# Kernel optimization log

Hardware: AMD Instinct MI355X
Metric: run time of the kernel (lower is better)

Reference implementation:

```python
import jax, jax.numpy as jnp
import numpy as np
from jax import lax

V, D, H, L = 128, 1024, 1024, 2
B, T = 64, 512


def setup_inputs() -> dict:
    key = jax.random.key(0)
    ks = jax.random.split(key, 8)
    s = 0.05
    return {
        "x": jax.random.randint(ks[0], (B, T), 0, V),
        "embed": jax.random.normal(ks[1], (V, D), jnp.float32) * s,
        "Wx": jax.random.normal(ks[2], (L, 4 * H, D), jnp.float32) * s,
        "Wh": jax.random.normal(ks[3], (L, 4 * H, H), jnp.float32) * s,
        "b": jax.random.normal(ks[4], (L, 4 * H), jnp.float32) * s,
        "Wout": jax.random.normal(ks[5], (V, H), jnp.float32) * s,
        "bout": jax.random.normal(ks[6], (V,), jnp.float32) * s,
    }


def _lstm_step(Wx, Wh, b, carry, x_t):
    # carry: (h[L,B,H], c[L,B,H]); x_t: [B,D]
    h, c = carry
    inp = x_t
    hs, cs = [], []
    for l in range(L):
        gates = inp @ Wx[l].T + h[l] @ Wh[l].T + b[l]  # [B,4H]
        i, f, g, o = jnp.split(gates, 4, axis=-1)
        c_new = jax.nn.sigmoid(f) * c[l] + jax.nn.sigmoid(i) * jnp.tanh(g)
        h_new = jax.nn.sigmoid(o) * jnp.tanh(c_new)
        hs.append(h_new)
        cs.append(c_new)
        inp = h_new
    return (jnp.stack(hs), jnp.stack(cs)), inp


def reference(x, embed, Wx, Wh, b, Wout, bout):
    emb = embed[x]                      # [B,T,D]
    xs = jnp.swapaxes(emb, 0, 1)        # [T,B,D] for scan over time
    h0 = jnp.zeros((L, B, H), emb.dtype)
    c0 = jnp.zeros((L, B, H), emb.dtype)
    step = lambda carry, x_t: _lstm_step(Wx, Wh, b, carry, x_t)
    _, outs = lax.scan(step, (h0, c0), xs)  # outs: [T,B,H] (top-layer h)
    outs = jnp.swapaxes(outs, 0, 1)         # [B,T,H]
    logits = outs @ Wout.T + bout           # [B,T,V]
    return logits
```

## Files before the change

kernel.cpp:

```cpp
#include <hip/hip_runtime.h>
#include <hip/hip_bf16.h>

constexpr int cV = 128, cD = 1024, cH = 1024, cB = 64, cT = 512;
constexpr int c4H = 4096;
constexpr int NBLK = 256;
constexpr int FSTR = 32;

typedef __attribute__((ext_vector_type(8))) short bf16x8;
typedef __attribute__((ext_vector_type(4))) float f32x4;
typedef __attribute__((ext_vector_type(4))) int i32x4;

__device__ __forceinline__ short f2b(float f) {
  __hip_bfloat16 h = __float2bfloat16(f);
  return __builtin_bit_cast(short, h);
}
__device__ __forceinline__ float sigf(float x) { return 1.0f / (1.0f + __expf(-x)); }

__device__ __forceinline__ void gload16(const short* g, short* l) {
  __builtin_amdgcn_global_load_lds(
      (const __attribute__((address_space(1))) void*)g,
      (__attribute__((address_space(3))) void*)l, 16, 0, 0);
}

__global__ void cvt_bf16_kernel(const float* __restrict__ src, short* __restrict__ dst, int n8) {
  int q = blockIdx.x * blockDim.x + threadIdx.x;
  if (q >= n8) return;
  const float4* s = (const float4*)src + (size_t)q * 2;
  float4 a = s[0], b = s[1];
  union { short s8[8]; int4 v; } u;
  u.s8[0] = f2b(a.x); u.s8[1] = f2b(a.y); u.s8[2] = f2b(a.z); u.s8[3] = f2b(a.w);
  u.s8[4] = f2b(b.x); u.s8[5] = f2b(b.y); u.s8[6] = f2b(b.z); u.s8[7] = f2b(b.w);
  *(int4*)(dst + (size_t)q * 8) = u.v;
}

struct RParams {
  const float* Wx;
  const float* Wh;
  const float* bias;
  const int*   x;
  const short* embedb;
  short* h0hist;
  short* outs;
  const short* zpage;
  int* flags;
};

__launch_bounds__(512, 1)
__global__ void lstm_recurrent(RParams P) {
  __shared__ __align__(16) short S0[32768];
  __shared__ __align__(16) short S1[32768];
  __shared__ float pLDS[8][32][17];
  __shared__ float cLDS[512];
  __shared__ float bLDS[2][32];
  __shared__ short hLDS[512];

  const int tid = threadIdx.x;
  const int lane = tid & 63, wv = tid >> 6;
  const int l15 = lane & 15, lhi = lane >> 4;
  const int op = wv & 3;
  const int ns = wv >> 2;
  const int blk = blockIdx.x;
  const int slice = blk & 127;
  const int bh = blk >> 7;
  const int hc0 = slice * 8;
  int* F = P.flags;
  const int fbase = bh * 128;

  bf16x8 w[32];
  {
    const float* Wsrc = ((op & 1) ? P.Wh : P.Wx) + (size_t)(op >> 1) * c4H * cD;
    int r = ns * 16 + l15;
    const float* base = Wsrc + (size_t)((r >> 3) * cH + hc0 + (r & 7)) * cD + lhi * 8;
    #pragma unroll
    for (int kt = 0; kt < 32; ++kt) {
      float4 a = *(const float4*)(base + kt * 32);
      float4 b = *(const float4*)(base + kt * 32 + 4);
      union { short s8[8]; bf16x8 v; } u;
      u.s8[0] = f2b(a.x); u.s8[1] = f2b(a.y); u.s8[2] = f2b(a.z); u.s8[3] = f2b(a.w);
      u.s8[4] = f2b(b.x); u.s8[5] = f2b(b.y); u.s8[6] = f2b(b.z); u.s8[7] = f2b(b.w);
      w[kt] = u.v;
    }
  }
  if (tid < 64) {
    int l = tid >> 5, r = tid & 31;
    bLDS[l][r] = P.bias[l * c4H + (r >> 3) * cH + hc0 + (r & 7)];
  }
  cLDS[tid] = 0.0f;
  __syncthreads();

  f32x4 accx[2] = {};
  if (op == 0) {
    int v0 = P.x[(bh * 32 + l15) * cT + 0];
    int v1 = P.x[(bh * 32 + 16 + l15) * cT + 0];
    const short* e0 = P.embedb + (size_t)v0 * 1024 + lhi * 8;
    const short* e1 = P.embedb + (size_t)v1 * 1024 + lhi * 8;
    #pragma unroll
    for (int kt = 0; kt < 32; ++kt) {
      bf16x8 a0 = *(const bf16x8*)(e0 + kt * 32);
      bf16x8 a1 = *(const bf16x8*)(e1 + kt * 32);
      accx[0] = __builtin_amdgcn_mfma_f32_16x16x32_bf16(a0, w[kt], accx[0], 0, 0, 0);
      accx[1] = __builtin_amdgcn_mfma_f32_16x16x32_bf16(a1, w[kt], accx[1], 0, 0, 0);
    }
  }

  for (int p = 0; p <= cT; ++p) {
    const bool l0act = (p < cT);
    const bool l1act = (p >= 1);
    const short* s0g = P.h0hist + (size_t)p * 65536;
    const short* s1g = (p >= 2) ? (P.outs + (size_t)(p - 2) * 65536) : P.zpage;

    if (wv >= 6) {
      const int* fa = &F[(fbase + 2 * lane) * FSTR];
      const int* fb = &F[(fbase + 2 * lane + 1) * FSTR];
      const short* gsrc = (wv == 7) ? s0g : s1g;
      short* ldst = (wv == 7) ? S0 : S1;
      unsigned long long staged = 0ull;
      while (staged != ~0ull) {
        int va = __hip_atomic_load(fa, __ATOMIC_RELAXED, __HIP_MEMORY_SCOPE_AGENT);
        int vb = __hip_atomic_load(fb, __ATOMIC_RELAXED, __HIP_MEMORY_SCOPE_AGENT);
        unsigned long long m = __ballot(va >= p && vb >= p) & ~staged;
        if (!m) { __builtin_amdgcn_s_sleep(1); continue; }
        staged |= m;
        while (m) {
          int c = __builtin_ctzll(m);
          m &= m - 1;
          int oct = 2 * c + (lane >> 5);
          int row = lane & 31;
          gload16(gsrc + oct * 512 + bh * 256 + row * 8, ldst + (c * 64 + lane) * 8);
        }
      }
      asm volatile("s_waitcnt vmcnt(0)" ::: "memory");
    }
    __syncthreads();

    f32x4 acc[2];
    if (op == 0) {
      acc[0] = accx[0]; acc[1] = accx[1];
    } else {
      acc[0] = (f32x4){0.f, 0.f, 0.f, 0.f};
      acc[1] = (f32x4){0.f, 0.f, 0.f, 0.f};
      const short* S = (op == 3) ? S1 : S0;
      const short* lb = S + lhi * 256 + l15 * 8;
      #pragma unroll
      for (int kt = 0; kt < 32; ++kt) {
        bf16x8 a0 = *(const bf16x8*)(lb + kt * 1024);
        bf16x8 a1 = *(const bf16x8*)(lb + kt * 1024 + 128);
        acc[0] = __builtin_amdgcn_mfma_f32_16x16x32_bf16(a0, w[kt], acc[0], 0, 0, 0);
        acc[1] = __builtin_amdgcn_mfma_f32_16x16x32_bf16(a1, w[kt], acc[1], 0, 0, 0);
      }
    }
    #pragma unroll
    for (int mi = 0; mi < 2; ++mi)
      #pragma unroll
      for (int v = 0; v < 4; ++v)
        pLDS[wv][mi * 16 + lhi * 4 + v][l15] = acc[mi][v];
    __syncthreads();

    {
      int l = tid >> 8, b = (tid >> 3) & 31, hc = tid & 7;
      bool act = l ? l1act : l0act;
      if (act) {
        float gt[4];
        #pragma unroll
        for (int g = 0; g < 4; ++g) {
          int r = g * 8 + hc;
          int wB = (r >> 4) * 4 + 2 * l;
          gt[g] = pLDS[wB][b][r & 15] + pLDS[wB + 1][b][r & 15] + bLDS[l][r];
        }
        float cold = cLDS[tid];
        float cn = sigf(gt[1]) * cold + sigf(gt[0]) * tanhf(gt[2]);
        float hn = sigf(gt[3]) * tanhf(cn);
        cLDS[tid] = cn;
        hLDS[tid] = f2b(hn);
      }
    }
    __syncthreads();

    if (wv == 0) {
      bool doStore = (lane < 32) ? l0act : l1act;
      if (doStore) {
        short* d = (lane < 32)
            ? (P.h0hist + (size_t)(p + 1) * 65536 + slice * 512 + bh * 256 + (lane & 31) * 8)
            : (P.outs   + (size_t)(p - 1) * 65536 + slice * 512 + bh * 256 + (lane & 31) * 8);
        i32x4 hv = *(const i32x4*)&hLDS[lane * 8];
        asm volatile("global_store_dwordx4 %0, %1, off sc0 sc1" :: "v"(d), "v"(hv) : "memory");
      }
      asm volatile("s_waitcnt vmcnt(0)" ::: "memory");
      if (lane == 0)
        __hip_atomic_store(&F[blk * FSTR], p + 1, __ATOMIC_RELAXED, __HIP_MEMORY_SCOPE_AGENT);
    }

    if (op == 0) {
      accx[0] = (f32x4){0.f, 0.f, 0.f, 0.f};
      accx[1] = (f32x4){0.f, 0.f, 0.f, 0.f};
      if (p + 1 < cT) {
        int t = p + 1;
        int v0 = P.x[(bh * 32 + l15) * cT + t];
        int v1 = P.x[(bh * 32 + 16 + l15) * cT + t];
        const short* e0 = P.embedb + (size_t)v0 * 1024 + lhi * 8;
        const short* e1 = P.embedb + (size_t)v1 * 1024 + lhi * 8;
        #pragma unroll
        for (int kt = 0; kt < 32; ++kt) {
          bf16x8 a0 = *(const bf16x8*)(e0 + kt * 32);
          bf16x8 a1 = *(const bf16x8*)(e1 + kt * 32);
          accx[0] = __builtin_amdgcn_mfma_f32_16x16x32_bf16(a0, w[kt], accx[0], 0, 0, 0);
          accx[1] = __builtin_amdgcn_mfma_f32_16x16x32_bf16(a1, w[kt], accx[1], 0, 0, 0);
        }
      }
    }
  }
}

__launch_bounds__(256, 1)
__global__ void proj_kernel(const short* __restrict__ outs, const short* __restrict__ Woutb,
                            const float* __restrict__ bout, float* __restrict__ logits) {
  const int tid = threadIdx.x, lane = tid & 63, wv = tid >> 6;
  const int l15 = lane & 15, lhi = lane >> 4;
  const int t = blockIdx.x;
  const int row = wv * 16 + l15;
  const short* Abase = outs + (size_t)t * 65536;
  f32x4 acc[8] = {};
  for (int k = 0; k < 1024; k += 32) {
    bf16x8 af = *(const bf16x8*)(Abase + ((k >> 3) + lhi) * 512 + row * 8);
    #pragma unroll
    for (int nn = 0; nn < 8; ++nn) {
      bf16x8 bf = *(const bf16x8*)(Woutb + (size_t)(nn * 16 + l15) * 1024 + k + lhi * 8);
      acc[nn] = __builtin_amdgcn_mfma_f32_16x16x32_bf16(af, bf, acc[nn], 0, 0, 0);
    }
  }
  #pragma unroll
  for (int nn = 0; nn < 8; ++nn) {
    #pragma unroll
    for (int v = 0; v < 4; ++v) {
      int b = wv * 16 + lhi * 4 + v;
      int col = nn * 16 + l15;
      logits[(size_t)b * (cT * cV) + (size_t)t * cV + col] = acc[nn][v] + bout[col];
    }
  }
}

extern "C" void kernel_launch(void* const* d_in, const int* in_sizes, int n_in,
                              void* d_out, int out_size, void* d_ws, size_t ws_size,
                              hipStream_t stream) {
  const int* x = (const int*)d_in[0];
  const float* embed = (const float*)d_in[1];
  const float* Wx = (const float*)d_in[2];
  const float* Wh = (const float*)d_in[3];
  const float* bias = (const float*)d_in[4];
  const float* Wout = (const float*)d_in[5];
  const float* bout = (const float*)d_in[6];
  float* logits = (float*)d_out;

  char* ws = (char*)d_ws;
  size_t off = 0;
  auto alloc = [&](size_t bytes) {
    char* p = ws + off;
    off += (bytes + 255) & ~(size_t)255;
    return p;
  };
  short* Woutb  = (short*)alloc((size_t)cV * cH * 2);
  short* embedb = (short*)alloc((size_t)cV * cD * 2);
  short* outs   = (short*)alloc((size_t)cT * 65536 * 2);
  short* h0hist = (short*)alloc((size_t)(cT + 1) * 65536 * 2);
  char* state0 = ws + off;
  short* zpage  = (short*)alloc((size_t)65536 * 2);
  int* flags    = (int*)alloc((size_t)NBLK * FSTR * sizeof(int));
  size_t state_bytes = (size_t)((ws + off) - state0);

  hipMemsetAsync(state0, 0, state_bytes, stream);
  hipMemsetAsync(h0hist, 0, (size_t)65536 * 2, stream);

  int n8 = cV * cH / 8;
  cvt_bf16_kernel<<<(n8 + 255) / 256, 256, 0, stream>>>(Wout, Woutb, n8);
  cvt_bf16_kernel<<<(n8 + 255) / 256, 256, 0, stream>>>(embed, embedb, n8);

  RParams P{Wx, Wh, bias, x, embedb, h0hist, outs, zpage, flags};
  lstm_recurrent<<<dim3(NBLK), dim3(512), 0, stream>>>(P);

  proj_kernel<<<cT, 256, 0, stream>>>(outs, Woutb, bout, logits);
}
```

Baseline: 4.220 ms.

## Spread h staging across all waves with per-chunk LDS progress flags

```diff
diff --git a/kernel.cpp b/kernel.cpp
--- a/kernel.cpp
+++ b/kernel.cpp
@@ -53,6 +53,7 @@
   __shared__ float cLDS[512];
   __shared__ float bLDS[2][32];
   __shared__ short hLDS[512];
+  __shared__ int prog[8];
 
   const int tid = threadIdx.x;
   const int lane = tid & 63, wv = tid >> 6;
@@ -86,67 +87,71 @@
     bLDS[l][r] = P.bias[l * c4H + (r >> 3) * cH + hc0 + (r & 7)];
   }
   cLDS[tid] = 0.0f;
+  if (tid < 8) prog[tid] = 0;
   __syncthreads();
-
-  f32x4 accx[2] = {};
-  if (op == 0) {
-    int v0 = P.x[(bh * 32 + l15) * cT + 0];
-    int v1 = P.x[(bh * 32 + 16 + l15) * cT + 0];
-    const short* e0 = P.embedb + (size_t)v0 * 1024 + lhi * 8;
-    const short* e1 = P.embedb + (size_t)v1 * 1024 + lhi * 8;
-    #pragma unroll
-    for (int kt = 0; kt < 32; ++kt) {
-      bf16x8 a0 = *(const bf16x8*)(e0 + kt * 32);
-      bf16x8 a1 = *(const bf16x8*)(e1 + kt * 32);
-      accx[0] = __builtin_amdgcn_mfma_f32_16x16x32_bf16(a0, w[kt], accx[0], 0, 0, 0);
-      accx[1] = __builtin_amdgcn_mfma_f32_16x16x32_bf16(a1, w[kt], accx[1], 0, 0, 0);
-    }
-  }
 
   for (int p = 0; p <= cT; ++p) {
     const bool l0act = (p < cT);
     const bool l1act = (p >= 1);
     const short* s0g = P.h0hist + (size_t)p * 65536;
     const short* s1g = (p >= 2) ? (P.outs + (size_t)(p - 2) * 65536) : P.zpage;
-
-    if (wv >= 6) {
-      const int* fa = &F[(fbase + 2 * lane) * FSTR];
-      const int* fb = &F[(fbase + 2 * lane + 1) * FSTR];
-      const short* gsrc = (wv == 7) ? s0g : s1g;
-      short* ldst = (wv == 7) ? S0 : S1;
-      unsigned long long staged = 0ull;
-      while (staged != ~0ull) {
-        int va = __hip_atomic_load(fa, __ATOMIC_RELAXED, __HIP_MEMORY_SCOPE_AGENT);
-        int vb = __hip_atomic_load(fb, __ATOMIC_RELAXED, __HIP_MEMORY_SCOPE_AGENT);
-        unsigned long long m = __ballot(va >= p && vb >= p) & ~staged;
-        if (!m) { __builtin_amdgcn_s_sleep(1); continue; }
-        staged |= m;
-        while (m) {
-          int c = __builtin_ctzll(m);
-          m &= m - 1;
-          int oct = 2 * c + (lane >> 5);
-          int row = lane & 31;
-          gload16(gsrc + oct * 512 + bh * 256 + row * 8, ldst + (c * 64 + lane) * 8);
-        }
-      }
-      asm volatile("s_waitcnt vmcnt(0)" ::: "memory");
-    }
-    __syncthreads();
-
-    f32x4 acc[2];
+    const int p16 = p << 4;
+
+    {
+      const int* fptr = &F[(fbase + (wv << 4) + (lane & 15)) * FSTR];
+      int done = 0;
+      while (done < 8) {
+        int fv = __hip_atomic_load(fptr, __ATOMIC_RELAXED, __HIP_MEMORY_SCOPE_AGENT);
+        unsigned long long bl = __ballot(fv >= p);
+        int pr = done;
+        while (pr < 8 && ((bl >> (2 * pr)) & 3ull) == 3ull) ++pr;
+        if (pr > done) {
+          for (int j = done; j < pr; ++j) {
+            int oct = (wv << 4) + 2 * j + (lane >> 5);
+            int row = lane & 31;
+            int seg = (((wv << 3) + j) << 6) + lane;
+            gload16(s0g + oct * 512 + bh * 256 + row * 8, S0 + seg * 8);
+            gload16(s1g + oct * 512 + bh * 256 + row * 8, S1 + seg * 8);
+          }
+          asm volatile("s_waitcnt vmcnt(0)" ::: "memory");
+          if (lane == 0) ((volatile int*)prog)[wv] = p16 + 2 * pr;
+          done = pr;
+        } else {
+          __builtin_amdgcn_s_sleep(1);
+        }
+      }
+    }
+
+    f32x4 acc[2] = {{0.f,0.f,0.f,0.f}, {0.f,0.f,0.f,0.f}};
     if (op == 0) {
-      acc[0] = accx[0]; acc[1] = accx[1];
+      if (p < cT) {
+        int v0 = P.x[(bh * 32 + l15) * cT + p];
+        int v1 = P.x[(bh * 32 + 16 + l15) * cT + p];
+        const short* e0 = P.embedb + (size_t)v0 * 1024 + lhi * 8;
+        const short* e1 = P.embedb + (size_t)v1 * 1024 + lhi * 8;
+        #pragma unroll
+        for (int kt = 0; kt < 32; ++kt) {
+          bf16x8 a0 = *(const bf16x8*)(e0 + kt * 32);
+          bf16x8 a1 = *(const bf16x8*)(e1 + kt * 32);
+          acc[0] = __builtin_amdgcn_mfma_f32_16x16x32_bf16(a0, w[kt], acc[0], 0, 0, 0);
+          acc[1] = __builtin_amdgcn_mfma_f32_16x16x32_bf16(a1, w[kt], acc[1], 0, 0, 0);
+        }
+      }
     } else {
-      acc[0] = (f32x4){0.f, 0.f, 0.f, 0.f};
-      acc[1] = (f32x4){0.f, 0.f, 0.f, 0.f};
       const short* S = (op == 3) ? S1 : S0;
       const short* lb = S + lhi * 256 + l15 * 8;
       #pragma unroll
-      for (int kt = 0; kt < 32; ++kt) {
-        bf16x8 a0 = *(const bf16x8*)(lb + kt * 1024);
-        bf16x8 a1 = *(const bf16x8*)(lb + kt * 1024 + 128);
-        acc[0] = __builtin_amdgcn_mfma_f32_16x16x32_bf16(a0, w[kt], acc[0], 0, 0, 0);
-        acc[1] = __builtin_amdgcn_mfma_f32_16x16x32_bf16(a1, w[kt], acc[1], 0, 0, 0);
+      for (int g = 0; g < 8; ++g) {
+        while (((volatile int*)prog)[g] < p16 + 16) __builtin_amdgcn_s_sleep(0);
+        #pragma unroll
+        for (int k4 = 0; k4 < 4; ++k4) {
+          constexpr int dummy = 0; (void)dummy;
+          int kt = g * 4 + k4;
+          bf16x8 a0 = *(const bf16x8*)(lb + kt * 1024);
+          bf16x8 a1 = *(const bf16x8*)(lb + kt * 1024 + 128);
+          acc[0] = __builtin_amdgcn_mfma_f32_16x16x32_bf16(a0, w[g * 4 + k4], acc[0], 0, 0, 0);
+          acc[1] = __builtin_amdgcn_mfma_f32_16x16x32_bf16(a1, w[g * 4 + k4], acc[1], 0, 0, 0);
+        }
       }
     }
     #pragma unroll
@@ -176,7 +181,7 @@
     }
     __syncthreads();
 
-    if (wv == 0) {
+    if (wv == 7) {
       bool doStore = (lane < 32) ? l0act : l1act;
       if (doStore) {
         short* d = (lane < 32)
@@ -188,25 +193,6 @@
       asm volatile("s_waitcnt vmcnt(0)" ::: "memory");
       if (lane == 0)
         __hip_atomic_store(&F[blk * FSTR], p + 1, __ATOMIC_RELAXED, __HIP_MEMORY_SCOPE_AGENT);
-    }
-
-    if (op == 0) {
-      accx[0] = (f32x4){0.f, 0.f, 0.f, 0.f};
-      accx[1] = (f32x4){0.f, 0.f, 0.f, 0.f};
-      if (p + 1 < cT) {
-        int t = p + 1;
-        int v0 = P.x[(bh * 32 + l15) * cT + t];
-        int v1 = P.x[(bh * 32 + 16 + l15) * cT + t];
-        const short* e0 = P.embedb + (size_t)v0 * 1024 + lhi * 8;
-        const short* e1 = P.embedb + (size_t)v1 * 1024 + lhi * 8;
-        #pragma unroll
-        for (int kt = 0; kt < 32; ++kt) {
-          bf16x8 a0 = *(const bf16x8*)(e0 + kt * 32);
-          bf16x8 a1 = *(const bf16x8*)(e1 + kt * 32);
-          accx[0] = __builtin_amdgcn_mfma_f32_16x16x32_bf16(a0, w[kt], accx[0], 0, 0, 0);
-          accx[1] = __builtin_amdgcn_mfma_f32_16x16x32_bf16(a1, w[kt], accx[1], 0, 0, 0);
-        }
-      }
     }
   }
 }
```

Result: no change. 4.219 ms (-0.0%).
